# Performance work log

Hardware: AMD Instinct MI355X
Metric: run time of the kernel (lower is better)

The kernel has to match this reference:

```python
import jax, jax.numpy as jnp
import numpy as np

DIM = 1536
HEADS = 12
HD = DIM // HEADS  # 128
EPS = 1e-6
SINK_SIZE = 1          # frames
MAX_ATTN = 1920        # tokens (sliding window)


def setup_inputs() -> dict:
    key = jax.random.key(0)
    ks = jax.random.split(key, 10)
    B = 1
    F, H, W = 8, 16, 24
    L = F * H * W  # 3072
    s = 0.02
    inp = {
        "x": jax.random.normal(ks[0], (B, L, DIM), jnp.float32),
        "seq_lens": jnp.array([L], jnp.int32),
        "grid_sizes": jnp.array([[F, H, W]], jnp.int32),
        "freqs": jax.random.normal(ks[1], (1024, HD // 2, 2), jnp.float32),
        "wq": jax.random.normal(ks[2], (DIM, DIM), jnp.float32) * s,
        "bq": jnp.zeros((DIM,), jnp.float32),
        "wk": jax.random.normal(ks[3], (DIM, DIM), jnp.float32) * s,
        "bk": jnp.zeros((DIM,), jnp.float32),
        "wv": jax.random.normal(ks[4], (DIM, DIM), jnp.float32) * s,
        "bv": jnp.zeros((DIM,), jnp.float32),
        "wo": jax.random.normal(ks[5], (DIM, DIM), jnp.float32) * s,
        "bo": jnp.zeros((DIM,), jnp.float32),
        "nq_w": jnp.ones((DIM,), jnp.float32),
        "nk_w": jnp.ones((DIM,), jnp.float32),
    }
    return inp


def _rmsnorm(x, w):
    # WanRMSNorm: x * rsqrt(mean(x^2) + eps) * weight
    return x * jax.lax.rsqrt(jnp.mean(x * x, axis=-1, keepdims=True) + EPS) * w


def _rope(x, F, H, W, fc):
    # x: [B, L, n, d]; fc: complex [1024, d//2]
    B, L, n, d = x.shape
    c = d // 2
    c1 = c - 2 * (c // 3)  # temporal split
    c2 = c // 3
    f0, f1, f2 = fc[:, :c1], fc[:, c1:c1 + c2], fc[:, c1 + c2:]
    fr = jnp.concatenate([
        jnp.broadcast_to(f0[:F, None, None, :], (F, H, W, c1)),
        jnp.broadcast_to(f1[None, :H, None, :], (F, H, W, c2)),
        jnp.broadcast_to(f2[None, None, :W, :], (F, H, W, c2)),
    ], axis=-1).reshape(L, 1, c)  # [L, 1, c]
    xp = x.reshape(B, L, n, c, 2)
    xc = jax.lax.complex(xp[..., 0], xp[..., 1])  # [B, L, n, c]
    xr = xc * fr[None]
    return jnp.stack([jnp.real(xr), jnp.imag(xr)], axis=-1).reshape(B, L, n, d)


def reference(x, seq_lens, grid_sizes, freqs, wq, bq, wk, bk, wv, bv, wo, bo, nq_w, nk_w):
    B, L, _ = x.shape
    gs = np.asarray(grid_sizes)[0]
    F, H, W = int(gs[0]), int(gs[1]), int(gs[2])
    fs = H * W  # frame_seqlen
    sink = SINK_SIZE * fs

    q = _rmsnorm(x @ wq.T + bq, nq_w).reshape(B, L, HEADS, HD)
    k = _rmsnorm(x @ wk.T + bk, nk_w).reshape(B, L, HEADS, HD)
    v = (x @ wv.T + bv).reshape(B, L, HEADS, HD)

    fc = jax.lax.complex(freqs[..., 0], freqs[..., 1])  # [1024, HD//2]
    q = _rope(q, F, H, W, fc)
    k = _rope(k, F, H, W, fc)

    # sink + windowed frame-causal block mask (flex_attention block_mask)
    idx = jnp.arange(L)
    qf = idx // fs
    kf = idx // fs
    mask = (kf[None, :] <= qf[:, None]) & (
        (idx[None, :] < sink) | (idx[None, :] >= (qf[:, None] + 1) * fs - MAX_ATTN)
    )  # [L, L]

    scale = 1.0 / np.float32(np.sqrt(HD))
    scores = jnp.einsum('bqnd,bknd->bnqk', q, k) * scale
    scores = jnp.where(mask[None, None], scores, jnp.float32(-1e30))
    attn = jax.nn.softmax(scores, axis=-1)
    out = jnp.einsum('bnqk,bknd->bqnd', attn, v).reshape(B, L, DIM)
    return out @ wo.T + bo
```

## Files before the change

### kernel.cpp

```cpp
#include <hip/hip_runtime.h>
#include <stdint.h>

#define DIMC 1536
#define LTOK 3072
#define HEADS 12
#define HD 128
#define FS 384
#define MAXATTN 1920
#define HTOK 1152
#define NHT 1920

typedef __attribute__((ext_vector_type(4))) float f32x4;
typedef __attribute__((ext_vector_type(8))) short bf16x8;
typedef __attribute__((ext_vector_type(4))) unsigned int u32x4;

__device__ __forceinline__ unsigned short f2bf(float f) {
  union { float f; unsigned int u; } c; c.f = f;
  unsigned int u = c.u + 0x7fffu + ((c.u >> 16) & 1u);
  return (unsigned short)(u >> 16);
}
__device__ __forceinline__ float bf2f(unsigned short s) {
  union { unsigned int u; float f; } c; c.u = (unsigned int)s << 16; return c.f;
}
__device__ __forceinline__ unsigned int cvtpk(float a, float b) {
  unsigned int r;
  asm("v_cvt_pk_bf16_f32 %0, %1, %2" : "=v"(r) : "v"(a), "v"(b));
  return r;
}

__device__ __forceinline__ void dma16(const void* g, void* l) {
  __builtin_amdgcn_global_load_lds(
      (const __attribute__((address_space(1))) unsigned int*)g,
      (__attribute__((address_space(3))) unsigned int*)l, 16, 0, 0);
}

__device__ __forceinline__ int vperm4(int G) {
  return (((G >> 3) & 1) << 3) | (((G >> 1) & 1) << 2) | ((G & 1) << 1) | ((G >> 2) & 1);
}

__global__ __launch_bounds__(256)
void cvt_all_k(const float* __restrict__ x, const float* __restrict__ wq,
               const float* __restrict__ wk, const float* __restrict__ wv,
               const float* __restrict__ wo,
               unsigned short* __restrict__ xb, unsigned short* __restrict__ wqb,
               unsigned short* __restrict__ wkb, unsigned short* __restrict__ wvb,
               unsigned short* __restrict__ wob)
{
  const int i = blockIdx.x * 256 + threadIdx.x;
  const int n0 = LTOK * DIMC / 4;
  const int nw = DIMC * DIMC / 4;
  const float* src; unsigned short* dst; int off;
  if (i < n0) { src = x; dst = xb; off = i; }
  else {
    int j = i - n0; int w = j / nw; off = j - w * nw;
    src = (w == 0) ? wq : (w == 1) ? wk : (w == 2) ? wv : wo;
    dst = (w == 0) ? wqb : (w == 1) ? wkb : (w == 2) ? wvb : wob;
  }
  float4 f = ((const float4*)src)[off];
  uint2 o;
  o.x = (unsigned int)f2bf(f.x) | ((unsigned int)f2bf(f.y) << 16);
  o.y = (unsigned int)f2bf(f.z) | ((unsigned int)f2bf(f.w) << 16);
  ((uint2*)dst)[off] = o;
}

__global__ __launch_bounds__(256)
void gemm_qkv(const unsigned short* __restrict__ A,
              const unsigned short* __restrict__ B0,
              const unsigned short* __restrict__ B1,
              const unsigned short* __restrict__ B2,
              const float* __restrict__ bias0,
              const float* __restrict__ bias1,
              const float* __restrict__ bias2,
              unsigned short* __restrict__ o0, unsigned short* __restrict__ o1,
              unsigned short* __restrict__ vt)
{
  const int z = blockIdx.z;
  const unsigned short* Bw = (z == 0) ? B0 : (z == 1) ? B1 : B2;
  const float* bias = (z == 0) ? bias0 : (z == 1) ? bias1 : bias2;

  __shared__ __align__(16) unsigned short lA[128 * 64];
  __shared__ __align__(16) unsigned short lB[128 * 64];

  const int tid = threadIdx.x;
  const int wave = tid >> 6;
  const int lane = tid & 63;
  const int m0 = blockIdx.y * 128;
  const int n0 = blockIdx.x * 128;
  const int wm = (wave >> 1) * 64;
  const int wn = (wave & 1) * 64;

  f32x4 acc[4][4] = {};

  const int srow = tid >> 3;
  const int scol = ((tid & 7) ^ (srow & 7)) * 8;
  const unsigned short* ga = A  + (size_t)(m0 + srow) * DIMC + scol;
  const unsigned short* gb = Bw + (size_t)(n0 + srow) * DIMC + scol;
  unsigned short* la = lA + tid * 8;
  unsigned short* lb = lB + tid * 8;

  const int fr = lane & 15;
  const int g = lane >> 4;
  const int fx = fr & 7;

  for (int k0 = 0; k0 < DIMC; k0 += 64) {
    dma16(ga + k0,                     la);
    dma16(ga + k0 + (size_t)32 * DIMC, la + 2048);
    dma16(ga + k0 + (size_t)64 * DIMC, la + 4096);
    dma16(ga + k0 + (size_t)96 * DIMC, la + 6144);
    dma16(gb + k0,                     lb);
    dma16(gb + k0 + (size_t)32 * DIMC, lb + 2048);
    dma16(gb + k0 + (size_t)64 * DIMC, lb + 4096);
    dma16(gb + k0 + (size_t)96 * DIMC, lb + 6144);
    __syncthreads();

#pragma unroll
    for (int kk = 0; kk < 2; ++kk) {
      const int cx = ((kk * 4 + g) ^ fx) * 8;
      bf16x8 af[4], bf[4];
#pragma unroll
      for (int i = 0; i < 4; ++i)
        af[i] = *(const bf16x8*)&lA[(wm + i * 16 + fr) * 64 + cx];
#pragma unroll
      for (int j = 0; j < 4; ++j)
        bf[j] = *(const bf16x8*)&lB[(wn + j * 16 + fr) * 64 + cx];
#pragma unroll
      for (int i = 0; i < 4; ++i)
#pragma unroll
        for (int j = 0; j < 4; ++j)
          acc[i][j] = __builtin_amdgcn_mfma_f32_16x16x32_bf16(af[i], bf[j], acc[i][j], 0, 0, 0);
    }
    __syncthreads();
  }

  const int col = lane & 15;
  const int rb = (lane >> 4) * 4;
  if (z < 2) {
    unsigned short* outp = z ? o1 : o0;
#pragma unroll
    for (int j = 0; j < 4; ++j) {
      const int gn = n0 + wn + j * 16 + col;
      const float bv = bias[gn];
#pragma unroll
      for (int i = 0; i < 4; ++i)
#pragma unroll
        for (int r = 0; r < 4; ++r) {
          const int gm = m0 + wm + i * 16 + rb + r;
          outp[(size_t)gm * DIMC + gn] = f2bf(acc[i][j][r] + bv);
        }
    }
  } else {
#pragma unroll
    for (int j = 0; j < 4; ++j) {
      const int gn = n0 + wn + j * 16 + col;
      const float bv = bias[gn];
#pragma unroll
      for (int i = 0; i < 4; ++i) {
        const int base = wm + i * 16 + rb;
        const int tile = base & ~63;
        const int toka = m0 + tile + vperm4((base & 63) >> 2) * 4;
        uint2 pk;
        pk.x = (unsigned int)f2bf(acc[i][j][0] + bv) |
               ((unsigned int)f2bf(acc[i][j][1] + bv) << 16);
        pk.y = (unsigned int)f2bf(acc[i][j][2] + bv) |
               ((unsigned int)f2bf(acc[i][j][3] + bv) << 16);
        *(uint2*)(vt + (size_t)gn * LTOK + toka) = pk;
      }
    }
  }
}

__global__ __launch_bounds__(256)
void gemm_wo(const unsigned short* __restrict__ A,
             const unsigned short* __restrict__ Bw,
             const float* __restrict__ bias,
             float* __restrict__ outp)
{
  __shared__ __align__(16) unsigned short lA[64 * 64];
  __shared__ __align__(16) unsigned short lB[128 * 64];

  const int tid = threadIdx.x;
  const int wave = tid >> 6;
  const int lane = tid & 63;
  const int m0 = blockIdx.y * 64;
  const int n0 = blockIdx.x * 128;
  const int wm = (wave >> 1) * 32;
  const int wn = (wave & 1) * 64;

  f32x4 acc[2][4] = {};

  const int srow = tid >> 3;
  const int scol = ((tid & 7) ^ (srow & 7)) * 8;
  const unsigned short* ga = A  + (size_t)(m0 + srow) * DIMC + scol;
  const unsigned short* gb = Bw + (size_t)(n0 + srow) * DIMC + scol;
  unsigned short* la = lA + tid * 8;
  unsigned short* lb = lB + tid * 8;

  const int fr = lane & 15;
  const int g = lane >> 4;
  const int fx = fr & 7;

  for (int k0 = 0; k0 < DIMC; k0 += 64) {
    dma16(ga + k0,                     la);
    dma16(ga + k0 + (size_t)32 * DIMC, la + 2048);
    dma16(gb + k0,                     lb);
    dma16(gb + k0 + (size_t)32 * DIMC, lb + 2048);
    dma16(gb + k0 + (size_t)64 * DIMC, lb + 4096);
    dma16(gb + k0 + (size_t)96 * DIMC, lb + 6144);
    __syncthreads();

#pragma unroll
    for (int kk = 0; kk < 2; ++kk) {
      const int cx = ((kk * 4 + g) ^ fx) * 8;
      bf16x8 af[2], bf[4];
#pragma unroll
      for (int i = 0; i < 2; ++i)
        af[i] = *(const bf16x8*)&lA[(wm + i * 16 + fr) * 64 + cx];
#pragma unroll
      for (int j = 0; j < 4; ++j)
        bf[j] = *(const bf16x8*)&lB[(wn + j * 16 + fr) * 64 + cx];
#pragma unroll
      for (int i = 0; i < 2; ++i)
#pragma unroll
        for (int j = 0; j < 4; ++j)
          acc[i][j] = __builtin_amdgcn_mfma_f32_16x16x32_bf16(af[i], bf[j], acc[i][j], 0, 0, 0);
    }
    __syncthreads();
  }

  const int col = lane & 15;
  const int rb = (lane >> 4) * 4;
#pragma unroll
  for (int j = 0; j < 4; ++j) {
    const int gn = n0 + wn + j * 16 + col;
    const float bv = bias[gn];
#pragma unroll
    for (int i = 0; i < 2; ++i)
#pragma unroll
      for (int r = 0; r < 4; ++r) {
        const int gm = m0 + wm + i * 16 + rb + r;
        outp[(size_t)gm * DIMC + gn] = acc[i][j][r] + bv;
      }
  }
}

__global__ __launch_bounds__(192)
void post_qkv_k(unsigned short* __restrict__ q, unsigned short* __restrict__ k,
                const float* __restrict__ nqw, const float* __restrict__ nkw,
                const float* __restrict__ freqs)
{
  const int bx = blockIdx.x;
  const int tid = threadIdx.x;
  const int which = bx >= LTOK;
  const int tok = bx - which * LTOK;
  unsigned short* row = (which ? k : q) + (size_t)tok * DIMC;
  const float* nw = which ? nkw : nqw;
  const float sc = which ? 1.f : (0.08838834764831845f * 1.4426950408889634f);
  const int base = tid * 8;

  const bf16x8 rv = *(const bf16x8*)(row + base);
  float vv[8];
  float ss = 0.f;
#pragma unroll
  for (int j = 0; j < 8; ++j) {
    vv[j] = bf2f((unsigned short)rv[j]);
    ss += vv[j] * vv[j];
  }
#pragma unroll
  for (int off = 1; off < 64; off <<= 1) ss += __shfl_xor(ss, off);
  __shared__ float wsum[3];
  if ((tid & 63) == 0) wsum[tid >> 6] = ss;
  __syncthreads();
  const float total = wsum[0] + wsum[1] + wsum[2];
  const float rms = rsqrtf(total * (1.f / DIMC) + 1e-6f);

  const int f = tok / FS;
  const int rem = tok - f * FS;
  const int h = rem / 24;
  const int w = rem - h * 24;

  float nwv[8];
  *(float4*)&nwv[0] = *(const float4*)(nw + base);
  *(float4*)&nwv[4] = *(const float4*)(nw + base + 4);

  u32x4 outp;
#pragma unroll
  for (int pp = 0; pp < 4; ++pp) {
    const int P = (base >> 1) + pp;
    const int p = P & 63;
    const int t = (p < 22) ? f : ((p < 43) ? h : w);
    const float2 fc = *(const float2*)(freqs + t * 128 + p * 2);
    const float e = vv[2 * pp]     * rms * nwv[2 * pp];
    const float o = vv[2 * pp + 1] * rms * nwv[2 * pp + 1];
    outp[pp] = (unsigned int)f2bf((e * fc.x - o * fc.y) * sc) |
               ((unsigned int)f2bf((e * fc.y + o * fc.x) * sc) << 16);
  }
  *(u32x4*)(row + base) = outp;
}

#define KBUF (64 * 128)
#define VBUF (128 * 64)
#define SLOTSZ (KBUF + VBUF)
__global__ __launch_bounds__(512)
void attn_flash(const unsigned short* __restrict__ q,
                const unsigned short* __restrict__ k,
                const unsigned short* __restrict__ vt,
                unsigned short* __restrict__ ab,
                float* __restrict__ Opart,
                float* __restrict__ mlbuf)
{
  const int bid = blockIdx.x;
  int qb, head, chunk, nch, tstart, tend;
  if (bid < 216)      { const int hb = bid >> 1; qb = 15 + hb / 12; head = hb % 12; chunk = bid & 1; nch = 2; tstart = chunk * 18; tend = tstart + 18; }
  else if (bid < 252) { const int b = bid - 216; qb = 6 + b / 12; head = b % 12; chunk = 0; nch = 1; tstart = 0; tend = 18; }
  else if (bid < 324) { const int b = bid - 252; const int hb = b >> 1; qb = 12 + hb / 12; head = hb % 12; chunk = b & 1; nch = 2; tstart = chunk ? 16 : 0; tend = chunk ? 30 : 16; }
  else if (bid < 396) { const int b = bid - 324; const int hb = b >> 1; qb = 9 + hb / 12; head = hb % 12; chunk = b & 1; nch = 2; tstart = chunk * 12; tend = tstart + 12; }
  else if (bid < 432) { const int b = bid - 396; qb = 3 + b / 12; head = b % 12; chunk = 0; nch = 1; tstart = 0; tend = 12; }
  else                { const int b = bid - 432; qb = b / 12;     head = b % 12; chunk = 0; nch = 1; tstart = 0; tend = 6; }

  const int q0 = qb * 128;
  const int qf = qb / 3;
  const int kend = (qf + 1) * FS;
  const int s2 = kend - MAXATTN;
  const bool two = (s2 > FS);
  const int nt1 = (two ? FS : kend) >> 6;

  const int tid = threadIdx.x;
  const int wave = tid >> 6, lane = tid & 63;
  const int col = lane & 15;
  const int g = lane >> 4;
  const int g4 = g * 4;

  __shared__ __align__(16) unsigned short Lds[3 * SLOTSZ];

  bf16x8 qfA[4];
  {
    const unsigned short* qr0 = q + (size_t)(q0 + wave * 16 + col) * DIMC + head * HD;
#pragma unroll
    for (int kk = 0; kk < 4; ++kk)
      qfA[kk] = *(const bf16x8*)(qr0 + kk * 32 + g * 8);
  }

  f32x4 o0[8] = {};
  float m0 = -3.0e38f, l0 = 0.f;

  const int krow = tid >> 4;
  const int kc8  = ((tid & 15) ^ (krow & 15)) * 8;
  const unsigned short* kg = k + (size_t)krow * DIMC + head * HD + kc8;
  const int vrow = tid >> 3;
  const int vc8  = ((tid & 7) ^ (vrow & 7)) * 8;
  const unsigned short* vg = vt + ((size_t)head * HD + vrow) * LTOK + vc8;

  auto stage = [&](int t, int slot) {
    const int kb = (t < nt1) ? t * 64 : s2 + (t - nt1) * 64;
    unsigned short* sb = Lds + slot * SLOTSZ;
    const unsigned short* kp = kg + (size_t)kb * DIMC;
    unsigned short* kl = sb + tid * 8;
    dma16(kp,                     kl);
    dma16(kp + (size_t)32 * DIMC, kl + 32 * 128);
    const unsigned short* vp = vg + kb;
    unsigned short* vl = sb + KBUF + tid * 8;
    dma16(vp,                     vl);
    dma16(vp + (size_t)64 * LTOK, vl + 64 * 64);
  };

  stage(tstart, 0);
  if (tstart + 1 < tend) stage(tstart + 1, 1);

  int slot = 0;
  for (int t = tstart; t < tend; ++t) {
    if (t + 1 < tend) asm volatile("s_waitcnt vmcnt(4)" ::: "memory");
    else              asm volatile("s_waitcnt vmcnt(0)" ::: "memory");
    __builtin_amdgcn_s_barrier();
    __builtin_amdgcn_sched_barrier(0);

    if (t + 2 < tend) {
      int s2n = slot + 2; if (s2n >= 3) s2n -= 3;
      stage(t + 2, s2n);
    }

    const unsigned short* Ks = Lds + slot * SLOTSZ;
    const unsigned short* Vs = Ks + KBUF;

    f32x4 sA[4] = {};
    __builtin_amdgcn_s_setprio(1);
#pragma unroll
    for (int kt = 0; kt < 4; ++kt) {
      const unsigned short* kr = Ks + (kt * 16 + col) * 128;
#pragma unroll
      for (int kk = 0; kk < 4; ++kk) {
        bf16x8 kfr = *(const bf16x8*)(kr + ((kk * 4 + g) ^ col) * 8);
        sA[kt] = __builtin_amdgcn_mfma_f32_16x16x32_bf16(kfr, qfA[kk], sA[kt], 0, 0, 0);
      }
    }
    __builtin_amdgcn_s_setprio(0);

    float mxa = fmaxf(fmaxf(sA[0][0], sA[0][1]), fmaxf(sA[0][2], sA[0][3]));
    float mxb = fmaxf(fmaxf(sA[1][0], sA[1][1]), fmaxf(sA[1][2], sA[1][3]));
    float mxc = fmaxf(fmaxf(sA[2][0], sA[2][1]), fmaxf(sA[2][2], sA[2][3]));
    float mxd = fmaxf(fmaxf(sA[3][0], sA[3][1]), fmaxf(sA[3][2], sA[3][3]));
    float mx = fmaxf(fmaxf(mxa, mxb), fmaxf(mxc, mxd));
    mx = fmaxf(mx, __shfl_xor(mx, 16));
    mx = fmaxf(mx, __shfl_xor(mx, 32));

    if (!__all(mx <= m0 + 8.f)) {
      const float mn = fmaxf(m0, mx);
      const float al = exp2f(m0 - mn);
      m0 = mn;
      l0 *= al;
#pragma unroll
      for (int dt = 0; dt < 8; ++dt) o0[dt] *= al;
    }

    float p[16];
#pragma unroll
    for (int kt = 0; kt < 4; ++kt)
#pragma unroll
      for (int r = 0; r < 4; ++r)
        p[kt * 4 + r] = exp2f(sA[kt][r] - m0);

    float rs = ((p[0] + p[1]) + (p[2] + p[3])) + ((p[4] + p[5]) + (p[6] + p[7]))
             + ((p[8] + p[9]) + (p[10] + p[11])) + ((p[12] + p[13]) + (p[14] + p[15]));
    rs += __shfl_xor(rs, 16);
    rs += __shfl_xor(rs, 32);
    l0 += rs;

    u32x4 tA0, tA1;
    tA0[0] = cvtpk(p[0], p[1]);   tA0[1] = cvtpk(p[2], p[3]);
    tA0[2] = cvtpk(p[4], p[5]);   tA0[3] = cvtpk(p[6], p[7]);
    tA1[0] = cvtpk(p[8], p[9]);   tA1[1] = cvtpk(p[10], p[11]);
    tA1[2] = cvtpk(p[12], p[13]); tA1[3] = cvtpk(p[14], p[15]);
    const bf16x8 pfA0 = __builtin_bit_cast(bf16x8, tA0);
    const bf16x8 pfA1 = __builtin_bit_cast(bf16x8, tA1);

    const int vx0 = (g ^ (col & 7)) * 8;
    const int vx1 = ((4 + g) ^ (col & 7)) * 8;
    __builtin_amdgcn_s_setprio(1);
#pragma unroll
    for (int dt = 0; dt < 8; ++dt) {
      const unsigned short* vr = Vs + (dt * 16 + col) * 64;
      bf16x8 vf0 = *(const bf16x8*)(vr + vx0);
      o0[dt] = __builtin_amdgcn_mfma_f32_16x16x32_bf16(vf0, pfA0, o0[dt], 0, 0, 0);
      bf16x8 vf1 = *(const bf16x8*)(vr + vx1);
      o0[dt] = __builtin_amdgcn_mfma_f32_16x16x32_bf16(vf1, pfA1, o0[dt], 0, 0, 0);
    }
    __builtin_amdgcn_s_setprio(0);

    slot = (slot + 1 == 3) ? 0 : slot + 1;
  }

  const int qrow0 = q0 + wave * 16 + col;
  if (nch == 1) {
    const float i0 = 1.f / l0;
    unsigned short* or0 = ab + (size_t)qrow0 * DIMC + head * HD;
#pragma unroll
    for (int dt = 0; dt < 8; ++dt) {
      uint2 pk;
      pk.x = (unsigned int)f2bf(o0[dt][0] * i0) | ((unsigned int)f2bf(o0[dt][1] * i0) << 16);
      pk.y = (unsigned int)f2bf(o0[dt][2] * i0) | ((unsigned int)f2bf(o0[dt][3] * i0) << 16);
      *(uint2*)(or0 + dt * 16 + g4) = pk;
    }
  } else {
    const int tokp0 = qrow0 - HTOK;
    float* ob0 = Opart + ((size_t)(chunk * NHT + tokp0) * HEADS + head) * HD;
#pragma unroll
    for (int dt = 0; dt < 8; ++dt)
      *(f32x4*)(ob0 + dt * 16 + g4) = o0[dt];
    if (lane < 16) {
      float* mlp0 = mlbuf + 2 * ((size_t)(chunk * NHT + tokp0) * HEADS + head);
      mlp0[0] = m0; mlp0[1] = l0;
    }
  }
}

__global__ __launch_bounds__(384)
void merge_k(const float* __restrict__ Opart, const float* __restrict__ mlbuf,
             unsigned short* __restrict__ ab)
{
  const int tokp = blockIdx.x;
  const int tid = threadIdx.x;
  const int e = tid * 4;
  const int head = e >> 7;
  const size_t r0 = (size_t)tokp * DIMC + e;
  float4 o0 = *(const float4*)(Opart + r0);
  float4 o1 = *(const float4*)(Opart + (size_t)NHT * DIMC + r0);
  const float* ml0 = mlbuf + 2 * ((size_t)tokp * HEADS + head);
  const float* ml1 = mlbuf + 2 * ((size_t)(NHT + tokp) * HEADS + head);
  const float m0 = ml0[0], l0 = ml0[1], m1 = ml1[0], l1 = ml1[1];
  const float mm = fmaxf(m0, m1);
  const float a0 = exp2f(m0 - mm), a1 = exp2f(m1 - mm);
  const float inv = 1.f / (l0 * a0 + l1 * a1);
  uint2 pk;
  pk.x = (unsigned int)f2bf((o0.x * a0 + o1.x * a1) * inv) |
         ((unsigned int)f2bf((o0.y * a0 + o1.y * a1) * inv) << 16);
  pk.y = (unsigned int)f2bf((o0.z * a0 + o1.z * a1) * inv) |
         ((unsigned int)f2bf((o0.w * a0 + o1.w * a1) * inv) << 16);
  *(uint2*)(ab + (size_t)(HTOK + tokp) * DIMC + e) = pk;
}

extern "C" void kernel_launch(void* const* d_in, const int* in_sizes, int n_in,
                              void* d_out, int out_size, void* d_ws, size_t ws_size,
                              hipStream_t stream)
{
  (void)in_sizes; (void)n_in; (void)out_size; (void)ws_size;
  const float* x     = (const float*)d_in[0];
  const float* freqs = (const float*)d_in[3];
  const float* wq    = (const float*)d_in[4];
  const float* bq    = (const float*)d_in[5];
  const float* wk    = (const float*)d_in[6];
  const float* bk    = (const float*)d_in[7];
  const float* wv    = (const float*)d_in[8];
  const float* bv    = (const float*)d_in[9];
  const float* wo    = (const float*)d_in[10];
  const float* bo    = (const float*)d_in[11];
  const float* nqw   = (const float*)d_in[12];
  const float* nkw   = (const float*)d_in[13];

  char* ws = (char*)d_ws;
  size_t off = 0;
  auto take = [&](size_t bytes) -> void* {
    void* p = ws + off; off += (bytes + 255) & ~(size_t)255; return p;
  };
  unsigned short* wob = (unsigned short*)take((size_t)DIMC * DIMC * 2);
  unsigned short* qb  = (unsigned short*)take((size_t)LTOK * DIMC * 2);
  unsigned short* kb  = (unsigned short*)take((size_t)LTOK * DIMC * 2);
  unsigned short* vb  = (unsigned short*)take((size_t)LTOK * DIMC * 2);
  unsigned short* ab  = (unsigned short*)take((size_t)LTOK * DIMC * 2);
  unsigned short* vtb = (unsigned short*)take((size_t)LTOK * DIMC * 2);
  unsigned short* xb  = (unsigned short*)take((size_t)LTOK * DIMC * 2);
  unsigned short* wqb = (unsigned short*)take((size_t)DIMC * DIMC * 2);
  unsigned short* wkb = (unsigned short*)take((size_t)DIMC * DIMC * 2);
  unsigned short* wvb = (unsigned short*)take((size_t)DIMC * DIMC * 2);
  float* mlb = (float*)take((size_t)2 * NHT * HEADS * 2 * sizeof(float));
  float* Opart = (float*)xb;
  (void)vb;

  cvt_all_k<<<dim3(13824), dim3(256), 0, stream>>>(x, wq, wk, wv, wo,
                                                   xb, wqb, wkb, wvb, wob);

  gemm_qkv<<<dim3(DIMC / 128, LTOK / 128, 3), dim3(256), 0, stream>>>(
      xb, wqb, wkb, wvb, bq, bk, bv, qb, kb, vtb);

  post_qkv_k<<<dim3(2 * LTOK), dim3(192), 0, stream>>>(qb, kb, nqw, nkw, freqs);

  attn_flash<<<dim3(468), dim3(512), 0, stream>>>(qb, kb, vtb, ab, Opart, mlb);
  merge_k<<<dim3(NHT), dim3(384), 0, stream>>>(Opart, mlb, ab);

  gemm_wo<<<dim3(DIMC / 128, LTOK / 64), dim3(256), 0, stream>>>(
      ab, wob, bo, (float*)d_out);
}
```

Baseline: 283.3 us.

## Software-pipeline QK^T one tile ahead with a four-slot LDS ring buffer

The attention loop now computes the score MFMAs for tile t+1 while it runs the softmax and PV MFMAs for tile t. This lets the exp/max work overlap with matrix-core work. The LDS ring grows from three to four slots, and prefetch depth grows to three tiles, with adjusted vmcnt waits. The s_setprio hints are removed. The larger LDS footprint and extra live score registers may reduce occupancy.

```diff
diff --git a/kernel.cpp b/kernel.cpp
--- a/kernel.cpp
+++ b/kernel.cpp
@@ -330,7 +330,7 @@
   const int g = lane >> 4;
   const int g4 = g * 4;
 
-  __shared__ __align__(16) unsigned short Lds[3 * SLOTSZ];
+  __shared__ __align__(16) unsigned short Lds[4 * SLOTSZ];
 
   bf16x8 qfA[4];
   {
@@ -363,41 +363,50 @@
     dma16(vp + (size_t)64 * LTOK, vl + 64 * 64);
   };
 
-  stage(tstart, 0);
-  if (tstart + 1 < tend) stage(tstart + 1, 1);
+  stage(tstart,     0);
+  stage(tstart + 1, 1);
+  stage(tstart + 2, 2);
+  asm volatile("s_waitcnt vmcnt(8)" ::: "memory");
+  __builtin_amdgcn_s_barrier();
+
+  f32x4 sc[4] = {};
+#pragma unroll
+  for (int kt = 0; kt < 4; ++kt) {
+    const unsigned short* kr = Lds + (kt * 16 + col) * 128;
+#pragma unroll
+    for (int kk = 0; kk < 4; ++kk) {
+      bf16x8 kfr = *(const bf16x8*)(kr + ((kk * 4 + g) ^ col) * 8);
+      sc[kt] = __builtin_amdgcn_mfma_f32_16x16x32_bf16(kfr, qfA[kk], sc[kt], 0, 0, 0);
+    }
+  }
 
   int slot = 0;
   for (int t = tstart; t < tend; ++t) {
-    if (t + 1 < tend) asm volatile("s_waitcnt vmcnt(4)" ::: "memory");
+    if (t + 2 < tend) asm volatile("s_waitcnt vmcnt(4)" ::: "memory");
     else              asm volatile("s_waitcnt vmcnt(0)" ::: "memory");
     __builtin_amdgcn_s_barrier();
-    __builtin_amdgcn_sched_barrier(0);
-
-    if (t + 2 < tend) {
-      int s2n = slot + 2; if (s2n >= 3) s2n -= 3;
-      stage(t + 2, s2n);
-    }
-
-    const unsigned short* Ks = Lds + slot * SLOTSZ;
-    const unsigned short* Vs = Ks + KBUF;
-
-    f32x4 sA[4] = {};
-    __builtin_amdgcn_s_setprio(1);
-#pragma unroll
-    for (int kt = 0; kt < 4; ++kt) {
-      const unsigned short* kr = Ks + (kt * 16 + col) * 128;
-#pragma unroll
-      for (int kk = 0; kk < 4; ++kk) {
-        bf16x8 kfr = *(const bf16x8*)(kr + ((kk * 4 + g) ^ col) * 8);
-        sA[kt] = __builtin_amdgcn_mfma_f32_16x16x32_bf16(kfr, qfA[kk], sA[kt], 0, 0, 0);
+
+    const int sl1 = (slot + 1) & 3;
+    if (t + 3 < tend) stage(t + 3, (slot + 3) & 3);
+
+    f32x4 sn[4] = {};
+    if (t + 1 < tend) {
+      const unsigned short* Kn = Lds + sl1 * SLOTSZ;
+#pragma unroll
+      for (int kt = 0; kt < 4; ++kt) {
+        const unsigned short* kr = Kn + (kt * 16 + col) * 128;
+#pragma unroll
+        for (int kk = 0; kk < 4; ++kk) {
+          bf16x8 kfr = *(const bf16x8*)(kr + ((kk * 4 + g) ^ col) * 8);
+          sn[kt] = __builtin_amdgcn_mfma_f32_16x16x32_bf16(kfr, qfA[kk], sn[kt], 0, 0, 0);
+        }
       }
     }
-    __builtin_amdgcn_s_setprio(0);
-
-    float mxa = fmaxf(fmaxf(sA[0][0], sA[0][1]), fmaxf(sA[0][2], sA[0][3]));
-    float mxb = fmaxf(fmaxf(sA[1][0], sA[1][1]), fmaxf(sA[1][2], sA[1][3]));
-    float mxc = fmaxf(fmaxf(sA[2][0], sA[2][1]), fmaxf(sA[2][2], sA[2][3]));
-    float mxd = fmaxf(fmaxf(sA[3][0], sA[3][1]), fmaxf(sA[3][2], sA[3][3]));
+
+    float mxa = fmaxf(fmaxf(sc[0][0], sc[0][1]), fmaxf(sc[0][2], sc[0][3]));
+    float mxb = fmaxf(fmaxf(sc[1][0], sc[1][1]), fmaxf(sc[1][2], sc[1][3]));
+    float mxc = fmaxf(fmaxf(sc[2][0], sc[2][1]), fmaxf(sc[2][2], sc[2][3]));
+    float mxd = fmaxf(fmaxf(sc[3][0], sc[3][1]), fmaxf(sc[3][2], sc[3][3]));
     float mx = fmaxf(fmaxf(mxa, mxb), fmaxf(mxc, mxd));
     mx = fmaxf(mx, __shfl_xor(mx, 16));
     mx = fmaxf(mx, __shfl_xor(mx, 32));
@@ -416,7 +425,7 @@
     for (int kt = 0; kt < 4; ++kt)
 #pragma unroll
       for (int r = 0; r < 4; ++r)
-        p[kt * 4 + r] = exp2f(sA[kt][r] - m0);
+        p[kt * 4 + r] = exp2f(sc[kt][r] - m0);
 
     float rs = ((p[0] + p[1]) + (p[2] + p[3])) + ((p[4] + p[5]) + (p[6] + p[7]))
              + ((p[8] + p[9]) + (p[10] + p[11])) + ((p[12] + p[13]) + (p[14] + p[15]));
@@ -432,9 +441,9 @@
     const bf16x8 pfA0 = __builtin_bit_cast(bf16x8, tA0);
     const bf16x8 pfA1 = __builtin_bit_cast(bf16x8, tA1);
 
+    const unsigned short* Vs = Lds + slot * SLOTSZ + KBUF;
     const int vx0 = (g ^ (col & 7)) * 8;
     const int vx1 = ((4 + g) ^ (col & 7)) * 8;
-    __builtin_amdgcn_s_setprio(1);
 #pragma unroll
     for (int dt = 0; dt < 8; ++dt) {
       const unsigned short* vr = Vs + (dt * 16 + col) * 64;
@@ -443,9 +452,9 @@
       bf16x8 vf1 = *(const bf16x8*)(vr + vx1);
       o0[dt] = __builtin_amdgcn_mfma_f32_16x16x32_bf16(vf1, pfA1, o0[dt], 0, 0, 0);
     }
-    __builtin_amdgcn_s_setprio(0);
-
-    slot = (slot + 1 == 3) ? 0 : slot + 1;
+
+    sc[0] = sn[0]; sc[1] = sn[1]; sc[2] = sn[2]; sc[3] = sn[3];
+    slot = sl1;
   }
 
   const int qrow0 = q0 + wave * 16 + col;
```

New measurement: 282.9 us. Within noise of the previous version (-0.2%).
